# Kernel optimization log

Hardware: AMD Instinct MI355X
Metric: run time of the kernel (lower is better)

## Reference

```python
import jax, jax.numpy as jnp
import numpy as np
from jax import lax

N_HEADS = 12
HEAD_DIM = 64
ALPHA = 4.0  # spikingjelly surrogate.Sigmoid default alpha
EPS = 1e-5   # BatchNorm1d default eps

@jax.custom_vjp
def _heaviside(v):
    return (v >= 0.0).astype(v.dtype)

def _heaviside_fwd(v):
    return _heaviside(v), v

def _heaviside_bwd(v, g):
    sg = jax.nn.sigmoid(ALPHA * v)
    return (g * ALPHA * sg * (1.0 - sg),)

_heaviside.defvjp(_heaviside_fwd, _heaviside_bwd)

def if_node(x):
    """Multi-step IFNode (v_threshold=1, hard reset to 0), scan over leading T dim."""
    def step(v, xt):
        v = v + xt                      # integrate
        s = _heaviside(v - 1.0)         # fire
        v = (1.0 - s) * v               # hard reset: spiked neurons -> 0
        return v, s
    _, spikes = lax.scan(step, jnp.zeros_like(x[0]), x)
    return spikes

def bn1d(x):
    """Fresh (training-mode) BatchNorm1d over (T, S, D) with channels=S;
    affine weight=1, bias=0 at init, so pure normalization over axes (0,2)."""
    mean = x.mean(axis=(0, 2), keepdims=True)
    var = x.var(axis=(0, 2), keepdims=True)  # biased variance, as torch BN uses
    return (x - mean) * lax.rsqrt(var + EPS)

def setup_inputs() -> dict:
    key = jax.random.key(0)
    ks = jax.random.split(key, 5)
    T, S, D = 4, 2048, 768
    x = jax.random.normal(ks[0], (T, S, D), dtype=jnp.float32)
    scale = 0.02
    wq = jax.random.normal(ks[1], (D, D), dtype=jnp.float32) * scale
    wk = jax.random.normal(ks[2], (D, D), dtype=jnp.float32) * scale
    wv = jax.random.normal(ks[3], (D, D), dtype=jnp.float32) * scale
    wo = jax.random.normal(ks[4], (D, D), dtype=jnp.float32) * scale
    return {"x": x, "wq": wq, "wk": wk, "wv": wv, "wo": wo, "cur_pos": S}

def reference(x, wq, wk, wv, wo, cur_pos):
    T, S, D = x.shape
    tmp = if_node(x)                    # init_spike
    Q = tmp @ wq
    V = tmp @ wv
    K = tmp @ wk
    Q = if_node(bn1d(Q))                # spike_q(bnq(Q))
    V = if_node(bn1d(V))                # spike_v(bnv(V))
    K = if_node(bn1d(K))                # spike_k(bnk(K))
    # (T, S, H, hd) -> (T, H, S, hd)
    Qh = Q.reshape(T, S, N_HEADS, HEAD_DIM).transpose(0, 2, 1, 3)
    Vh = V.reshape(T, S, N_HEADS, HEAD_DIM).transpose(0, 2, 1, 3)
    Kh = K.reshape(T, S, N_HEADS, HEAD_DIM).transpose(0, 2, 1, 3)
    QK = (Qh * Kh).sum(axis=2, keepdims=True)   # (T, H, 1, hd)
    QK = if_node(QK)                    # talking_heads
    QKV = Vh * QK                       # (T, H, S, hd)
    QKV = QKV.transpose(0, 2, 1, 3).reshape(T, S, D)
    return bn1d(QKV @ wo)
```

## Files before the change

kernel.cpp:

```cpp
#include <hip/hip_runtime.h>

#define T_ 4
#define S_ 2048
#define D_ 768
#define SD_ (S_ * D_)
#define TSD_ (T_ * SD_)
#define H_ 12
#define HD_ 64
#define PLANE_BYTES 2359296u

typedef int int32x4 __attribute__((ext_vector_type(4)));

__device__ __forceinline__ void cp16(unsigned char* lds, const unsigned char* g) {
    __builtin_amdgcn_global_load_lds(
        (const __attribute__((address_space(1))) unsigned int*)g,
        (__attribute__((address_space(3))) unsigned int*)lds, 16, 0, 0);
}

__global__ __launch_bounds__(256) void k_prep_w(const float* __restrict__ wq,
                                                const float* __restrict__ wk,
                                                const float* __restrict__ wv,
                                                const float* __restrict__ wo,
                                                unsigned char* __restrict__ Bp) {
    const float* W = (blockIdx.y == 0) ? wq : (blockIdx.y == 1) ? wk
                   : (blockIdx.y == 2) ? wv : wo;
    unsigned char* out = Bp + (size_t)blockIdx.y * PLANE_BYTES;
    int idx = blockIdx.x * 256 + threadIdx.x;
    int j0 = idx & 3;
    int lane = (idx >> 2) & 63;
    int kb = (idx >> 8) % 12;
    int rest = (idx >> 8) / 12;
    int nbg = rest % 48;
    int p = rest / 48;
    int n = nbg * 16 + (lane & 15);
    int kbase = kb * 64 + (lane >> 4) * 16 + j0 * 4;
    unsigned int packed = 0;
#pragma unroll
    for (int jj = 0; jj < 4; jj++) {
        float w = W[(size_t)(kbase + jj) * D_ + n];
        int u = (int)rintf(w * 1073741824.0f);
        for (int i = 0; i < p; i++) u = (u + 128) >> 8;
        packed |= ((unsigned int)(u & 255)) << (8 * jj);
    }
    *(unsigned int*)(out + (size_t)idx * 4) = packed;
}

__global__ __launch_bounds__(256) void k_ifnode_x(const float* __restrict__ x,
                                                  unsigned char* __restrict__ As) {
    int i = blockIdx.x * blockDim.x + threadIdx.x;
    int idx = i * 4;
    if (idx >= SD_) return;
    double v[4] = {0.0, 0.0, 0.0, 0.0};
#pragma unroll
    for (int t = 0; t < T_; t++) {
        float4 xt = *(const float4*)(x + (size_t)t * SD_ + idx);
        float xs[4] = {xt.x, xt.y, xt.z, xt.w};
        uchar4 sp;
        unsigned char* so = &sp.x;
#pragma unroll
        for (int j = 0; j < 4; j++) {
            v[j] += (double)xs[j];
            unsigned char s = (v[j] >= 1.0) ? 1 : 0;
            so[j] = s;
            if (s) v[j] = 0.0;
        }
        *(uchar4*)(As + (size_t)t * SD_ + idx) = sp;
    }
}

#define LDSBUF 24576

__global__ __launch_bounds__(256, 2) void k_gemm_i8(
    const unsigned char* __restrict__ A,
    const unsigned char* __restrict__ Bp,
    float* __restrict__ C0, float* __restrict__ C1, float* __restrict__ C2,
    int bzoff) {
    int z = blockIdx.z;
    const unsigned char* B = Bp + (size_t)(bzoff + z) * PLANE_BYTES;
    float* C = (z == 0) ? C0 : (z == 1) ? C1 : C2;

    __shared__ __align__(16) unsigned char smem[2 * LDSBUF];

    int tid = threadIdx.x;
    int lane = tid & 63;
    int w = tid >> 6;
    int row0 = blockIdx.x * 128;
    int n0 = blockIdx.y * 64;
    int nbg0 = blockIdx.y * 4;
    int col = lane & 15;
    int quad = lane >> 4;

    int32x4 zerov = {0, 0, 0, 0};
    int32x4 acc[2][4][4];
#pragma unroll
    for (int mb = 0; mb < 2; mb++)
#pragma unroll
        for (int nb = 0; nb < 4; nb++)
#pragma unroll
            for (int p = 0; p < 4; p++) acc[mb][nb][p] = zerov;

    const unsigned char* gA0 = A + (size_t)(row0 + (2 * w) * 16 + (lane >> 2)) * D_
                                 + (lane & 3) * 16;
    const unsigned char* gA1 = gA0 + (size_t)16 * D_;

    auto stage = [&](int buf, int kb) {
        unsigned char* ab = smem + buf * LDSBUF;
        cp16(ab + (2 * w + 0) * 1024, gA0 + kb * 64);
        cp16(ab + (2 * w + 1) * 1024, gA1 + kb * 64);
        unsigned char* bb = ab + 8192;
#pragma unroll
        for (int qi = 0; qi < 4; qi++) {
            int q = 4 * w + qi;
            int p = q >> 2, nb = q & 3;
            const unsigned char* gB =
                B + ((size_t)((p * 48 + nbg0 + nb) * 12 + kb) * 64 + lane) * 16;
            cp16(bb + q * 1024, gB);
        }
    };

    stage(0, 0);
    __syncthreads();

    for (int kb = 0; kb < 12; kb++) {
        int cur = kb & 1;
        if (kb < 11) stage(1 - cur, kb + 1);
        const unsigned char* ab = smem + cur * LDSBUF;
        int32x4 a0 = *(const int32x4*)(ab + (w * 32 + col) * 64 + quad * 16);
        int32x4 a1 = *(const int32x4*)(ab + (w * 32 + 16 + col) * 64 + quad * 16);
        const unsigned char* bb = ab + 8192;
#pragma unroll
        for (int p = 0; p < 4; p++)
#pragma unroll
            for (int nb = 0; nb < 4; nb++) {
                int32x4 bf = *(const int32x4*)(bb + ((p * 4 + nb) * 64 + lane) * 16);
                acc[0][nb][p] = __builtin_amdgcn_mfma_i32_16x16x64_i8(
                    a0, bf, acc[0][nb][p], 0, 0, 0);
                acc[1][nb][p] = __builtin_amdgcn_mfma_i32_16x16x64_i8(
                    a1, bf, acc[1][nb][p], 0, 0, 0);
            }
        __syncthreads();
    }

#pragma unroll
    for (int mb = 0; mb < 2; mb++)
#pragma unroll
        for (int nb = 0; nb < 4; nb++)
#pragma unroll
            for (int r = 0; r < 4; r++) {
                long t = (long)acc[mb][nb][0][r] + ((long)acc[mb][nb][1][r] << 8)
                       + ((long)acc[mb][nb][2][r] << 16)
                       + ((long)acc[mb][nb][3][r] << 24);
                float v = (float)((double)t * (1.0 / 1073741824.0));
                int rr = row0 + w * 32 + mb * 16 + quad * 4 + r;
                int cc = n0 + nb * 16 + col;
                C[(size_t)rr * D_ + cc] = v;
            }
}

__global__ __launch_bounds__(256) void k_bn_if(float* __restrict__ Q,
                                               float* __restrict__ Kt,
                                               float* __restrict__ Vf,
                                               unsigned char* __restrict__ Vs) {
    int s = blockIdx.x;
    int y = blockIdx.y;
    float* X = (y == 0) ? Q : (y == 1) ? Kt : Vf;

    __shared__ float buf[T_][D_];
    __shared__ double red[16];

    int tid = threadIdx.x;
    double sum = 0.0, sumsq = 0.0;
#pragma unroll
    for (int t = 0; t < T_; t++) {
        for (int d = tid; d < D_; d += 256) {
            float v = X[(size_t)t * SD_ + (size_t)s * D_ + d];
            buf[t][d] = v;
            double dv = (double)v;
            sum += dv;
            sumsq += dv * dv;
        }
    }
#pragma unroll
    for (int off = 32; off > 0; off >>= 1) {
        sum += __shfl_down(sum, off);
        sumsq += __shfl_down(sumsq, off);
    }
    int lane = tid & 63, wv = tid >> 6;
    if (lane == 0) { red[wv] = sum; red[4 + wv] = sumsq; }
    __syncthreads();
    if (tid == 0) {
        double s4 = red[0] + red[1] + red[2] + red[3];
        double q4 = red[4] + red[5] + red[6] + red[7];
        double mean = s4 / 3072.0;
        double var = q4 / 3072.0 - mean * mean;
        red[8] = mean;
        red[9] = 1.0 / sqrt(var + 1e-5);
    }
    __syncthreads();
    double mean = red[8], rstd = red[9];
    for (int d = tid; d < D_; d += 256) {
        double v = 0.0;
#pragma unroll
        for (int t = 0; t < T_; t++) {
            double xn = ((double)buf[t][d] - mean) * rstd;
            v += xn;
            int sp = (v >= 1.0) ? 1 : 0;
            if (y == 2)
                Vs[(size_t)t * SD_ + (size_t)s * D_ + d] = (unsigned char)sp;
            else
                X[(size_t)t * SD_ + (size_t)s * D_ + d] = (float)sp;
            if (sp) v = 0.0;
        }
    }
}

__global__ __launch_bounds__(256) void k_qk(const float* __restrict__ Q,
                                            const float* __restrict__ K,
                                            float* __restrict__ QK) {
    int b = blockIdx.x;
    int ch = b & 15;
    int th = b >> 4;
    int t = th / H_;
    int h = th % H_;
    int d = threadIdx.x & 63;
    int sg = threadIdx.x >> 6;
    const float* qb = Q + (size_t)t * SD_ + h * HD_ + d;
    const float* kb = K + (size_t)t * SD_ + h * HD_ + d;
    int s0 = ch * 128;
    float acc = 0.f;
    for (int s = s0 + sg; s < s0 + 128; s += 4)
        acc += qb[(size_t)s * D_] * kb[(size_t)s * D_];
    __shared__ float part[4][64];
    part[sg][d] = acc;
    __syncthreads();
    if (sg == 0) {
        float r = part[0][d] + part[1][d] + part[2][d] + part[3][d];
        atomicAdd(&QK[t * D_ + h * HD_ + d], r);
    }
}

__global__ __launch_bounds__(256) void k_form(const float* __restrict__ QK,
                                              unsigned char* __restrict__ As) {
    int i = blockIdx.x * 256 + threadIdx.x;
    int idx = i * 4;
    if (idx >= TSD_) return;
    int t = idx / SD_;
    int d = idx % D_;
    uchar4 a = *(const uchar4*)(As + idx);
    unsigned char* ap = &a.x;
#pragma unroll
    for (int j = 0; j < 4; j++) {
        float v = 0.f;
        float sp = 0.f;
        for (int tt = 0; tt <= t; tt++) {
            v += QK[tt * D_ + d + j];
            sp = (v >= 1.0f) ? 1.0f : 0.0f;
            if (sp > 0.f) v = 0.f;
        }
        ap[j] = (sp > 0.f) ? ap[j] : 0;
    }
    *(uchar4*)(As + idx) = a;
}

__global__ __launch_bounds__(256) void k_bn_out(const float* __restrict__ Xin,
                                                float* __restrict__ out) {
    int s = blockIdx.x;
    __shared__ float buf[T_][D_];
    __shared__ double red[16];
    int tid = threadIdx.x;
    double sum = 0.0, sumsq = 0.0;
#pragma unroll
    for (int t = 0; t < T_; t++) {
        for (int d = tid; d < D_; d += 256) {
            float v = Xin[(size_t)t * SD_ + (size_t)s * D_ + d];
            buf[t][d] = v;
            double dv = (double)v;
            sum += dv;
            sumsq += dv * dv;
        }
    }
#pragma unroll
    for (int off = 32; off > 0; off >>= 1) {
        sum += __shfl_down(sum, off);
        sumsq += __shfl_down(sumsq, off);
    }
    int lane = tid & 63, wv = tid >> 6;
    if (lane == 0) { red[wv] = sum; red[4 + wv] = sumsq; }
    __syncthreads();
    if (tid == 0) {
        double s4 = red[0] + red[1] + red[2] + red[3];
        double q4 = red[4] + red[5] + red[6] + red[7];
        double mean = s4 / 3072.0;
        double var = q4 / 3072.0 - mean * mean;
        red[8] = mean;
        red[9] = 1.0 / sqrt(var + 1e-5);
    }
    __syncthreads();
    double mean = red[8], rstd = red[9];
    for (int d = tid; d < D_; d += 256) {
#pragma unroll
        for (int t = 0; t < T_; t++) {
            double v = (double)buf[t][d];
            out[(size_t)t * SD_ + (size_t)s * D_ + d] =
                (float)((v - mean) * rstd);
        }
    }
}

extern "C" void kernel_launch(void* const* d_in, const int* in_sizes, int n_in,
                              void* d_out, int out_size, void* d_ws,
                              size_t ws_size, hipStream_t stream) {
    const float* x  = (const float*)d_in[0];
    const float* wq = (const float*)d_in[1];
    const float* wk = (const float*)d_in[2];
    const float* wv = (const float*)d_in[3];
    const float* wo = (const float*)d_in[4];
    float* out = (float*)d_out;

    float* ws  = (float*)d_ws;
    float* Qf  = ws;
    float* Kf  = ws + (size_t)TSD_;
    float* Vf  = ws + (size_t)2 * TSD_;
    float* QK  = ws + (size_t)3 * TSD_;
    float* QKs = QK + T_ * D_;
    unsigned char* As = (unsigned char*)(QKs + T_ * D_);
    unsigned char* Bp = As + (size_t)TSD_;

    hipMemsetAsync(QK, 0, T_ * D_ * sizeof(float), stream);
    k_prep_w<<<dim3(589824 / 256, 4), 256, 0, stream>>>(wq, wk, wv, wo, Bp);
    k_ifnode_x<<<SD_ / (4 * 256), 256, 0, stream>>>(x, As);
    k_gemm_i8<<<dim3(64, 12, 3), 256, 0, stream>>>(As, Bp, Qf, Kf, Vf, 0);
    k_bn_if<<<dim3(S_, 3), 256, 0, stream>>>(Qf, Kf, Vf, As);
    k_qk<<<T_ * H_ * 16, 256, 0, stream>>>(Qf, Kf, QK);
    k_form<<<TSD_ / (4 * 256), 256, 0, stream>>>(QK, As);
    k_gemm_i8<<<dim3(64, 12, 1), 256, 0, stream>>>(As, Bp, Qf, Qf, Qf, 3);
    k_bn_out<<<S_, 256, 0, stream>>>(Qf, out);
}
```

Before: 240.9 us.

## Fold talking-heads mask into GEMM, byte spikes for Q/K, retile warps 2x2

Q and K spikes are now written as bytes instead of floats, and the QK reduction works on packed 4-byte ANDs. The per-element k_form pass over the whole activation tensor is replaced by a tiny per-(t,d) IF kernel that produces a mask. The output GEMM applies that mask to its A fragments in registers. The GEMM warp tiling changes from 4x1 to 2x2, which gives each warp 4 A fragments and 2 B fragments, reducing LDS reads per MFMA. Costs are more accumulator registers and an extra mask load per k-step.

Result: faster. 228.0 us (-5.4%).

```diff
diff --git a/kernel.cpp b/kernel.cpp
--- a/kernel.cpp
+++ b/kernel.cpp
@@ -73,6 +73,7 @@
 __global__ __launch_bounds__(256, 2) void k_gemm_i8(
     const unsigned char* __restrict__ A,
     const unsigned char* __restrict__ Bp,
+    const unsigned char* __restrict__ Ms,
     float* __restrict__ C0, float* __restrict__ C1, float* __restrict__ C2,
     int bzoff) {
     int z = blockIdx.z;
@@ -84,18 +85,21 @@
     int tid = threadIdx.x;
     int lane = tid & 63;
     int w = tid >> 6;
+    int wm = w >> 1;
+    int wn = w & 1;
     int row0 = blockIdx.x * 128;
+    int tI = row0 >> 11;
     int n0 = blockIdx.y * 64;
     int nbg0 = blockIdx.y * 4;
     int col = lane & 15;
     int quad = lane >> 4;
 
     int32x4 zerov = {0, 0, 0, 0};
-    int32x4 acc[2][4][4];
-#pragma unroll
-    for (int mb = 0; mb < 2; mb++)
-#pragma unroll
-        for (int nb = 0; nb < 4; nb++)
+    int32x4 acc[4][2][4];
+#pragma unroll
+    for (int mb = 0; mb < 4; mb++)
+#pragma unroll
+        for (int nb = 0; nb < 2; nb++)
 #pragma unroll
             for (int p = 0; p < 4; p++) acc[mb][nb][p] = zerov;
 
@@ -125,45 +129,57 @@
         int cur = kb & 1;
         if (kb < 11) stage(1 - cur, kb + 1);
         const unsigned char* ab = smem + cur * LDSBUF;
-        int32x4 a0 = *(const int32x4*)(ab + (w * 32 + col) * 64 + quad * 16);
-        int32x4 a1 = *(const int32x4*)(ab + (w * 32 + 16 + col) * 64 + quad * 16);
+        int32x4 af[4];
+#pragma unroll
+        for (int mb = 0; mb < 4; mb++)
+            af[mb] = *(const int32x4*)(
+                ab + (wm * 64 + mb * 16 + col) * 64 + quad * 16);
+        if (Ms) {
+            int32x4 mv = *(const int32x4*)(Ms + tI * D_ + kb * 64 + quad * 16);
+#pragma unroll
+            for (int mb = 0; mb < 4; mb++) af[mb] &= mv;
+        }
         const unsigned char* bb = ab + 8192;
 #pragma unroll
         for (int p = 0; p < 4; p++)
 #pragma unroll
-            for (int nb = 0; nb < 4; nb++) {
-                int32x4 bf = *(const int32x4*)(bb + ((p * 4 + nb) * 64 + lane) * 16);
-                acc[0][nb][p] = __builtin_amdgcn_mfma_i32_16x16x64_i8(
-                    a0, bf, acc[0][nb][p], 0, 0, 0);
-                acc[1][nb][p] = __builtin_amdgcn_mfma_i32_16x16x64_i8(
-                    a1, bf, acc[1][nb][p], 0, 0, 0);
+            for (int nb = 0; nb < 2; nb++) {
+                int32x4 bf = *(const int32x4*)(
+                    bb + ((p * 4 + wn * 2 + nb) * 64 + lane) * 16);
+#pragma unroll
+                for (int mb = 0; mb < 4; mb++)
+                    acc[mb][nb][p] = __builtin_amdgcn_mfma_i32_16x16x64_i8(
+                        af[mb], bf, acc[mb][nb][p], 0, 0, 0);
             }
         __syncthreads();
     }
 
 #pragma unroll
-    for (int mb = 0; mb < 2; mb++)
-#pragma unroll
-        for (int nb = 0; nb < 4; nb++)
+    for (int mb = 0; mb < 4; mb++)
+#pragma unroll
+        for (int nb = 0; nb < 2; nb++)
 #pragma unroll
             for (int r = 0; r < 4; r++) {
                 long t = (long)acc[mb][nb][0][r] + ((long)acc[mb][nb][1][r] << 8)
                        + ((long)acc[mb][nb][2][r] << 16)
                        + ((long)acc[mb][nb][3][r] << 24);
                 float v = (float)((double)t * (1.0 / 1073741824.0));
-                int rr = row0 + w * 32 + mb * 16 + quad * 4 + r;
-                int cc = n0 + nb * 16 + col;
+                int rr = row0 + wm * 64 + mb * 16 + quad * 4 + r;
+                int cc = n0 + wn * 32 + nb * 16 + col;
                 C[(size_t)rr * D_ + cc] = v;
             }
 }
 
-__global__ __launch_bounds__(256) void k_bn_if(float* __restrict__ Q,
-                                               float* __restrict__ Kt,
-                                               float* __restrict__ Vf,
+__global__ __launch_bounds__(256) void k_bn_if(const float* __restrict__ Qf,
+                                               const float* __restrict__ Kf,
+                                               const float* __restrict__ Vf,
+                                               unsigned char* __restrict__ Qs,
+                                               unsigned char* __restrict__ Ks,
                                                unsigned char* __restrict__ Vs) {
     int s = blockIdx.x;
     int y = blockIdx.y;
-    float* X = (y == 0) ? Q : (y == 1) ? Kt : Vf;
+    const float* X = (y == 0) ? Qf : (y == 1) ? Kf : Vf;
+    unsigned char* Sp = (y == 0) ? Qs : (y == 1) ? Ks : Vs;
 
     __shared__ float buf[T_][D_];
     __shared__ double red[16];
@@ -205,61 +221,55 @@
             double xn = ((double)buf[t][d] - mean) * rstd;
             v += xn;
             int sp = (v >= 1.0) ? 1 : 0;
-            if (y == 2)
-                Vs[(size_t)t * SD_ + (size_t)s * D_ + d] = (unsigned char)sp;
-            else
-                X[(size_t)t * SD_ + (size_t)s * D_ + d] = (float)sp;
+            Sp[(size_t)t * SD_ + (size_t)s * D_ + d] = (unsigned char)sp;
             if (sp) v = 0.0;
         }
     }
 }
 
-__global__ __launch_bounds__(256) void k_qk(const float* __restrict__ Q,
-                                            const float* __restrict__ K,
+__global__ __launch_bounds__(256) void k_qk(const unsigned char* __restrict__ Qs,
+                                            const unsigned char* __restrict__ Ks,
                                             float* __restrict__ QK) {
     int b = blockIdx.x;
     int ch = b & 15;
     int th = b >> 4;
     int t = th / H_;
     int h = th % H_;
-    int d = threadIdx.x & 63;
-    int sg = threadIdx.x >> 6;
-    const float* qb = Q + (size_t)t * SD_ + h * HD_ + d;
-    const float* kb = K + (size_t)t * SD_ + h * HD_ + d;
+    int dq = threadIdx.x & 15;
+    int sl = threadIdx.x >> 4;
+    const unsigned int* qb = (const unsigned int*)(Qs + (size_t)t * SD_ + h * HD_);
+    const unsigned int* kb = (const unsigned int*)(Ks + (size_t)t * SD_ + h * HD_);
     int s0 = ch * 128;
-    float acc = 0.f;
-    for (int s = s0 + sg; s < s0 + 128; s += 4)
-        acc += qb[(size_t)s * D_] * kb[(size_t)s * D_];
-    __shared__ float part[4][64];
-    part[sg][d] = acc;
-    __syncthreads();
-    if (sg == 0) {
-        float r = part[0][d] + part[1][d] + part[2][d] + part[3][d];
-        atomicAdd(&QK[t * D_ + h * HD_ + d], r);
-    }
-}
-
-__global__ __launch_bounds__(256) void k_form(const float* __restrict__ QK,
-                                              unsigned char* __restrict__ As) {
-    int i = blockIdx.x * 256 + threadIdx.x;
-    int idx = i * 4;
-    if (idx >= TSD_) return;
-    int t = idx / SD_;
-    int d = idx % D_;
-    uchar4 a = *(const uchar4*)(As + idx);
-    unsigned char* ap = &a.x;
-#pragma unroll
-    for (int j = 0; j < 4; j++) {
-        float v = 0.f;
-        float sp = 0.f;
-        for (int tt = 0; tt <= t; tt++) {
-            v += QK[tt * D_ + d + j];
-            sp = (v >= 1.0f) ? 1.0f : 0.0f;
-            if (sp > 0.f) v = 0.f;
-        }
-        ap[j] = (sp > 0.f) ? ap[j] : 0;
-    }
-    *(uchar4*)(As + idx) = a;
+    unsigned int acc = 0;
+    for (int s = s0 + sl; s < s0 + 128; s += 16)
+        acc += (qb[s * 192 + dq] & kb[s * 192 + dq]);
+    __shared__ unsigned int part[16][16];
+    part[sl][dq] = acc;
+    __syncthreads();
+    if (sl == 0) {
+        unsigned int tot = 0;
+#pragma unroll
+        for (int i = 0; i < 16; i++) tot += part[i][dq];
+#pragma unroll
+        for (int j = 0; j < 4; j++) {
+            float v = (float)((tot >> (8 * j)) & 255u);
+            atomicAdd(&QK[t * D_ + h * HD_ + dq * 4 + j], v);
+        }
+    }
+}
+
+__global__ __launch_bounds__(256) void k_if_qk(const float* __restrict__ QK,
+                                               unsigned char* __restrict__ QKm) {
+    int j = blockIdx.x * 256 + threadIdx.x;
+    if (j >= D_) return;
+    float v = 0.f;
+#pragma unroll
+    for (int t = 0; t < T_; t++) {
+        v += QK[t * D_ + j];
+        unsigned char sp = (v >= 1.0f) ? 1 : 0;
+        QKm[t * D_ + j] = sp;
+        if (sp) v = 0.f;
+    }
 }
 
 __global__ __launch_bounds__(256) void k_bn_out(const float* __restrict__ Xin,
@@ -322,17 +332,21 @@
     float* Kf  = ws + (size_t)TSD_;
     float* Vf  = ws + (size_t)2 * TSD_;
     float* QK  = ws + (size_t)3 * TSD_;
-    float* QKs = QK + T_ * D_;
-    unsigned char* As = (unsigned char*)(QKs + T_ * D_);
-    unsigned char* Bp = As + (size_t)TSD_;
+    unsigned char* QKm = (unsigned char*)(QK + T_ * D_);
+    unsigned char* Sx  = QKm + 4096;
+    unsigned char* Ks  = Sx + (size_t)TSD_;
+    unsigned char* Vs  = Ks + (size_t)TSD_;
+    unsigned char* Bp  = Vs + (size_t)TSD_;
+    unsigned char* Qs  = Sx;
 
     hipMemsetAsync(QK, 0, T_ * D_ * sizeof(float), stream);
     k_prep_w<<<dim3(589824 / 256, 4), 256, 0, stream>>>(wq, wk, wv, wo, Bp);
-    k_ifnode_x<<<SD_ / (4 * 256), 256, 0, stream>>>(x, As);
-    k_gemm_i8<<<dim3(64, 12, 3), 256, 0, stream>>>(As, Bp, Qf, Kf, Vf, 0);
-    k_bn_if<<<dim3(S_, 3), 256, 0, stream>>>(Qf, Kf, Vf, As);
-    k_qk<<<T_ * H_ * 16, 256, 0, stream>>>(Qf, Kf, QK);
-    k_form<<<TSD_ / (4 * 256), 256, 0, stream>>>(QK, As);
-    k_gemm_i8<<<dim3(64, 12, 1), 256, 0, stream>>>(As, Bp, Qf, Qf, Qf, 3);
+    k_ifnode_x<<<SD_ / (4 * 256), 256, 0, stream>>>(x, Sx);
+    k_gemm_i8<<<dim3(64, 12, 3), 256, 0, stream>>>(Sx, Bp, nullptr,
+                                                   Qf, Kf, Vf, 0);
+    k_bn_if<<<dim3(S_, 3), 256, 0, stream>>>(Qf, Kf, Vf, Qs, Ks, Vs);
+    k_qk<<<T_ * H_ * 16, 256, 0, stream>>>(Qs, Ks, QK);
+    k_if_qk<<<3, 256, 0, stream>>>(QK, QKm);
+    k_gemm_i8<<<dim3(64, 12, 1), 256, 0, stream>>>(Vs, Bp, QKm, Qf, Qf, Qf, 3);
     k_bn_out<<<S_, 256, 0, stream>>>(Qf, out);
 }
```
